# Optimization experiments

Hardware: AMD Instinct MI355X
Metric: run time of the kernel (lower is better)

Reference implementation:

```python
import jax, jax.numpy as jnp
import numpy as np

R = 16
ALPHA = 32
SCALING = ALPHA / R  # 2.0


def setup_inputs() -> dict:
    key = jax.random.key(0)
    k_x, k_w, k_b, k_a, k_bm = jax.random.split(key, 5)
    d = 1024
    x = jax.random.normal(k_x, (4, 4096, d), dtype=jnp.float32)
    W = jax.random.normal(k_w, (d, d), dtype=jnp.float32) * 0.02
    b = jax.random.normal(k_b, (d,), dtype=jnp.float32) * 0.02
    A = jax.random.normal(k_a, (R, d), dtype=jnp.float32) * 0.02
    B = jax.random.normal(k_bm, (d, R), dtype=jnp.float32) * 0.02
    return {"x": x, "W": W, "b": b, "A": A, "B": B}


def reference(x, W, b, A, B):
    # base linear: x @ W^T + b   (W: [out, in])
    base = jnp.einsum("bsd,od->bso", x, W) + b
    # low-rank update: (x @ A^T) @ B^T, scaled (dropout p=0 -> identity)
    u = jnp.einsum("bsd,rd->bsr", x, A)   # [B, S, r]
    update = jnp.einsum("bsr,or->bso", u, B)
    return base + SCALING * update
```

## Files before the change

### kernel.cpp

```cpp
#include <hip/hip_runtime.h>


typedef __bf16 bf16x8 __attribute__((ext_vector_type(8)));
typedef float f32x4 __attribute__((ext_vector_type(4)));
typedef unsigned short ushort8 __attribute__((ext_vector_type(8)));

__device__ __forceinline__ unsigned short f2bf(float f) {
    __bf16 h = (__bf16)f;
    union { __bf16 b; unsigned short u; } v; v.b = h; return v.u;
}
__device__ __forceinline__ ushort8 cvt8u(f32x4 a, f32x4 b) {
    ushort8 o;
#pragma unroll
    for (int i = 0; i < 4; ++i) { o[i] = f2bf(a[i]); o[i + 4] = f2bf(b[i]); }
    return o;
}
__device__ __forceinline__ bf16x8 cvt8(f32x4 a, f32x4 b) {
    union { ushort8 u; bf16x8 h; } v; v.u = cvt8u(a, b); return v.h;
}
__device__ __forceinline__ void gld16(const void* g, void* l) {
    __builtin_amdgcn_global_load_lds(
        (const __attribute__((address_space(1))) unsigned int*)g,
        (__attribute__((address_space(3))) unsigned int*)l, 16, 0, 0);
}

#define FENCE() asm volatile("" ::: "memory")
#define BARRIER() do { FENCE(); __builtin_amdgcn_s_barrier(); FENCE(); } while (0)

__global__ __launch_bounds__(256) void prep(
    const float* __restrict__ W, const float* __restrict__ A,
    const float* __restrict__ B, unsigned short* __restrict__ Weff)
{
    const int idx = blockIdx.x * 256 + threadIdx.x;
    const int o  = idx >> 7;
    const int kc = (idx & 127) << 3;
    float br[16];
#pragma unroll
    for (int r = 0; r < 16; ++r) br[r] = 2.0f * B[o * 16 + r];
    float acc[8];
    const float* wrow = W + (size_t)o * 1024 + kc;
#pragma unroll
    for (int j = 0; j < 8; ++j) acc[j] = wrow[j];
#pragma unroll
    for (int r = 0; r < 16; ++r) {
        const float* arow = A + r * 1024 + kc;
#pragma unroll
        for (int j = 0; j < 8; ++j) acc[j] += br[r] * arow[j];
    }
    ushort8 o8;
#pragma unroll
    for (int j = 0; j < 8; ++j) o8[j] = f2bf(acc[j]);
    *(ushort8*)(Weff + (size_t)o * 1024 + kc) = o8;
}

__global__ __launch_bounds__(512, 4) void gemm256(
    const float* __restrict__ Xf,
    const unsigned short* __restrict__ Wt,
    const float* __restrict__ bias,
    float* __restrict__ out)
{
    extern __shared__ __align__(16) char lds[];

    const int t    = threadIdx.x;
    const int lane = t & 63;
    const int w    = t >> 6;
    const int wr   = w & 3;
    const int wc   = w >> 2;
    const int r16  = lane & 15;
    const int quad = lane >> 4;

    const int nwg = gridDim.x;
    int swz = blockIdx.x;
    if ((nwg & 7) == 0) swz = (swz & 7) * (nwg >> 3) + (swz >> 3);
    const int bm = (swz >> 2) * 128;
    const int bn = (swz & 3) * 256;

    const int ar = t >> 3;
    const int ac = (t & 7) ^ (ar & 7);
    const float* gA = Xf + (size_t)(bm + ar) * 1024 + ac * 4;
    const int adst = t * 16;

    const int brw = t >> 2;
    const int bcc = (t & 3) ^ ((brw >> 1) & 3);
    const unsigned short* pB0 = Wt + (size_t)(bn + brw) * 1024 + bcc * 8;
    const unsigned short* pB1 = pB0 + 131072;
    const int bdst = t * 16;

    const int o0 = ((2 * quad) ^ (r16 & 7)) * 16;
    const int o1 = ((2 * quad + 1) ^ (r16 & 7)) * 16;
    const int hA0 = ((wr * 2 + 0) * 16 + r16) * 128;
    const int hA1 = ((wr * 2 + 1) * 16 + r16) * 128;
    const int bB0 = 16384 + (wc * 16 + r16) * 64 + (quad ^ ((r16 >> 1) & 3)) * 16;

    f32x4 acc[2][8];
#pragma unroll
    for (int i = 0; i < 2; ++i)
#pragma unroll
        for (int jj = 0; jj < 8; ++jj)
            acc[i][jj] = (f32x4){0.f, 0.f, 0.f, 0.f};

#define STAGE_A(BUF, K)                                                        \
    do { gld16(gA + (K),             lds + (BUF) + adst);                      \
         gld16(gA + 65536 + (K),     lds + (BUF) + 8192 + adst);               \
         FENCE(); } while (0)
#define STAGE_B0(BUF, K) do { gld16(pB0 + (K), lds + (BUF) + 16384 + bdst); FENCE(); } while (0)
#define STAGE_B1(BUF, K) do { gld16(pB1 + (K), lds + (BUF) + 24576 + bdst); FENCE(); } while (0)

    STAGE_A(0, 0);
    STAGE_B0(0, 0);
    STAGE_B1(0, 0);
    STAGE_A(32768, 32);
    STAGE_B0(32768, 32);
    asm volatile("s_waitcnt vmcnt(3)" ::: "memory");
    BARRIER();

#pragma unroll 2
    for (int j = 0; j < 32; ++j) {
        const int cur = (j & 1) * 32768;
        const int nxt = cur ^ 32768;

        f32x4 a0l = *(const f32x4*)(lds + cur + hA0 + o0);
        f32x4 a0h = *(const f32x4*)(lds + cur + hA0 + o1);
        f32x4 a1l = *(const f32x4*)(lds + cur + hA1 + o0);
        f32x4 a1h = *(const f32x4*)(lds + cur + hA1 + o1);
        bf16x8 fb[4];
#pragma unroll
        for (int nt = 0; nt < 4; ++nt)
            fb[nt] = *(const bf16x8*)(lds + cur + bB0 + nt * 2048);
        if (j < 31) STAGE_B1(nxt, (j + 1) * 32);
        BARRIER();
        asm volatile("s_waitcnt lgkmcnt(0)" ::: "memory");
        __builtin_amdgcn_sched_barrier(0);
        __builtin_amdgcn_s_setprio(1);
        bf16x8 fa0 = cvt8(a0l, a0h), fa1 = cvt8(a1l, a1h);
#pragma unroll
        for (int nt = 0; nt < 4; ++nt) {
            acc[0][nt] = __builtin_amdgcn_mfma_f32_16x16x32_bf16(fa0, fb[nt], acc[0][nt], 0, 0, 0);
            acc[1][nt] = __builtin_amdgcn_mfma_f32_16x16x32_bf16(fa1, fb[nt], acc[1][nt], 0, 0, 0);
        }
        __builtin_amdgcn_s_setprio(0);
        BARRIER();

#pragma unroll
        for (int nt = 0; nt < 4; ++nt)
            fb[nt] = *(const bf16x8*)(lds + cur + bB0 + 8192 + nt * 2048);
        if (j < 30) { STAGE_A(cur, (j + 2) * 32); STAGE_B0(cur, (j + 2) * 32); }
        if (j < 30)       asm volatile("s_waitcnt vmcnt(3)" ::: "memory");
        else if (j == 30) asm volatile("s_waitcnt vmcnt(0)" ::: "memory");
        BARRIER();
        asm volatile("s_waitcnt lgkmcnt(0)" ::: "memory");
        __builtin_amdgcn_sched_barrier(0);
        __builtin_amdgcn_s_setprio(1);
#pragma unroll
        for (int nt = 0; nt < 4; ++nt) {
            acc[0][nt + 4] = __builtin_amdgcn_mfma_f32_16x16x32_bf16(fa0, fb[nt], acc[0][nt + 4], 0, 0, 0);
            acc[1][nt + 4] = __builtin_amdgcn_mfma_f32_16x16x32_bf16(fa1, fb[nt], acc[1][nt + 4], 0, 0, 0);
        }
        __builtin_amdgcn_s_setprio(0);
        BARRIER();
    }
#undef STAGE_A
#undef STAGE_B0
#undef STAGE_B1

    const int orow0 = bm + wr * 32 + quad * 4;
    const int ocol0 = bn + wc * 16 + r16;
#pragma unroll
    for (int nt = 0; nt < 8; ++nt) {
        const float bv = bias[ocol0 + nt * 32];
#pragma unroll
        for (int mt = 0; mt < 2; ++mt) {
            float* orow = out + (size_t)(orow0 + mt * 16) * 1024 + (ocol0 + nt * 32);
#pragma unroll
            for (int i = 0; i < 4; ++i)
                orow[(size_t)i * 1024] = acc[mt][nt][i] + bv;
        }
    }
}

template <bool XF32>
__global__ __launch_bounds__(256) void gemm_bt(
    const void* __restrict__ X_, const unsigned short* __restrict__ Wt,
    const float* __restrict__ bias, float* __restrict__ out)
{
    __shared__ __align__(16) unsigned short lA[128 * 32];
    __shared__ __align__(16) unsigned short lB[128 * 32];

    const int t    = threadIdx.x;
    const int lane = t & 63;
    const int w    = t >> 6;
    const int bm   = blockIdx.x * 128;
    const int bn   = blockIdx.y * 128;
    const int wm   = (w & 1) * 64;
    const int wn   = (w >> 1) * 64;
    const int r16  = lane & 15;
    const int quad = lane >> 4;

    const int srow = t >> 2;
    const int gc   = (t & 3) ^ ((srow >> 1) & 3);
    unsigned short* lsA = lA + t * 8;
    unsigned short* lsB = lB + t * 8;
    const size_t ga0 = (size_t)(bm + srow) * 1024 + gc * 8;
    const size_t ga1 = (size_t)(bm + srow + 64) * 1024 + gc * 8;
    const unsigned short* gB0 = Wt + (size_t)(bn + srow) * 1024 + gc * 8;

    const int p    = (quad ^ ((r16 >> 1) & 3)) * 8;
    const int aoff = (wm + r16) * 32 + p;
    const int boff = (wn + r16) * 32 + p;

    const unsigned short* Xb = (const unsigned short*)X_;
    const float*          Xf = (const float*)X_;

    f32x4 acc[4][4];
#pragma unroll
    for (int i = 0; i < 4; ++i)
#pragma unroll
        for (int j = 0; j < 4; ++j) {
            f32x4 z = {0.f, 0.f, 0.f, 0.f};
            acc[i][j] = z;
        }

    for (int kt = 0; kt < 1024; kt += 32) {
        if (XF32) {
            f32x4 a0 = *(const f32x4*)(Xf + ga0 + kt);
            f32x4 a1 = *(const f32x4*)(Xf + ga0 + kt + 4);
            f32x4 a2 = *(const f32x4*)(Xf + ga1 + kt);
            f32x4 a3 = *(const f32x4*)(Xf + ga1 + kt + 4);
            *(ushort8*)lsA          = cvt8u(a0, a1);
            *(ushort8*)(lsA + 2048) = cvt8u(a2, a3);
        } else {
            gld16(Xb + ga0 + kt, lsA);
            gld16(Xb + ga1 + kt, lsA + 2048);
        }
        gld16(gB0 + kt,             lsB);
        gld16(gB0 + kt + 64 * 1024, lsB + 2048);
        __syncthreads();

        bf16x8 fa[4], fb[4];
#pragma unroll
        for (int mt = 0; mt < 4; ++mt) fa[mt] = *(const bf16x8*)(lA + aoff + mt * 16 * 32);
#pragma unroll
        for (int nt = 0; nt < 4; ++nt) fb[nt] = *(const bf16x8*)(lB + boff + nt * 16 * 32);

#pragma unroll
        for (int mt = 0; mt < 4; ++mt)
#pragma unroll
            for (int nt = 0; nt < 4; ++nt)
                acc[mt][nt] = __builtin_amdgcn_mfma_f32_16x16x32_bf16(
                    fa[mt], fb[nt], acc[mt][nt], 0, 0, 0);

        __syncthreads();
    }

    const int orow0 = bm + wm + quad * 4;
    const int ocol0 = bn + wn + r16;
#pragma unroll
    for (int nt = 0; nt < 4; ++nt) {
        const float bv = bias[ocol0 + nt * 16];
#pragma unroll
        for (int mt = 0; mt < 4; ++mt)
#pragma unroll
            for (int i = 0; i < 4; ++i)
                out[(size_t)(orow0 + mt * 16 + i) * 1024 + (ocol0 + nt * 16)] =
                    acc[mt][nt][i] + bv;
    }
}

extern "C" void kernel_launch(void* const* d_in, const int* in_sizes, int n_in,
                              void* d_out, int out_size, void* d_ws, size_t ws_size,
                              hipStream_t stream) {
    const float* x  = (const float*)d_in[0];
    const float* W  = (const float*)d_in[1];
    const float* b  = (const float*)d_in[2];
    const float* A  = (const float*)d_in[3];
    const float* Bm = (const float*)d_in[4];
    float* out = (float*)d_out;

    const int M = in_sizes[0] / 1024;

    const bool fast = (ws_size >= (2u << 20) + 4096) && (M % 128 == 0);
    unsigned short* Weff = (unsigned short*)d_ws;
    hipLaunchKernelGGL(prep, dim3(512), dim3(256), 0, stream, W, A, Bm, Weff);
    if (fast) {
        hipLaunchKernelGGL(gemm256, dim3((M / 128) * 4), dim3(512), 65536, stream,
                           x, Weff, b, out);
    } else {
        hipLaunchKernelGGL((gemm_bt<true>), dim3(M / 128, 8), dim3(256), 0, stream,
                           (const void*)x, Weff, b, out);
    }
}
```

Baseline: 168.8 us.

## Pre-convert X to bf16 in prep kernel and retile GEMM to 128x128

The prep kernel now also converts the fp32 activations to bf16 in workspace. The GEMM then streams bf16 X through global-to-LDS loads with K-steps of 64 instead of converting fp32 on the fly. The GEMM tile changes from 128x256 to 128x128 with twice as many workgroups, and LDS fragment layout and swizzle are adjusted to match. This halves the X bytes read inside the GEMM and removes in-loop conversion. In exchange it adds an extra full pass over X (read fp32, write bf16) and reloads W tiles more often.

```diff
diff --git a/kernel.cpp b/kernel.cpp
--- a/kernel.cpp
+++ b/kernel.cpp
@@ -14,9 +14,6 @@
 #pragma unroll
     for (int i = 0; i < 4; ++i) { o[i] = f2bf(a[i]); o[i + 4] = f2bf(b[i]); }
     return o;
-}
-__device__ __forceinline__ bf16x8 cvt8(f32x4 a, f32x4 b) {
-    union { ushort8 u; bf16x8 h; } v; v.u = cvt8u(a, b); return v.h;
 }
 __device__ __forceinline__ void gld16(const void* g, void* l) {
     __builtin_amdgcn_global_load_lds(
@@ -28,33 +25,42 @@
 #define BARRIER() do { FENCE(); __builtin_amdgcn_s_barrier(); FENCE(); } while (0)
 
 __global__ __launch_bounds__(256) void prep(
-    const float* __restrict__ W, const float* __restrict__ A,
-    const float* __restrict__ B, unsigned short* __restrict__ Weff)
+    const float* __restrict__ X, const float* __restrict__ W,
+    const float* __restrict__ A, const float* __restrict__ B,
+    unsigned short* __restrict__ xbf, unsigned short* __restrict__ Weff)
 {
-    const int idx = blockIdx.x * 256 + threadIdx.x;
-    const int o  = idx >> 7;
-    const int kc = (idx & 127) << 3;
-    float br[16];
-#pragma unroll
-    for (int r = 0; r < 16; ++r) br[r] = 2.0f * B[o * 16 + r];
-    float acc[8];
-    const float* wrow = W + (size_t)o * 1024 + kc;
-#pragma unroll
-    for (int j = 0; j < 8; ++j) acc[j] = wrow[j];
-#pragma unroll
-    for (int r = 0; r < 16; ++r) {
-        const float* arow = A + r * 1024 + kc;
-#pragma unroll
-        for (int j = 0; j < 8; ++j) acc[j] += br[r] * arow[j];
-    }
-    ushort8 o8;
-#pragma unroll
-    for (int j = 0; j < 8; ++j) o8[j] = f2bf(acc[j]);
-    *(ushort8*)(Weff + (size_t)o * 1024 + kc) = o8;
+    const int b = blockIdx.x;
+    if (b < 512) {
+        const int idx = b * 256 + threadIdx.x;
+        const int o  = idx >> 7;
+        const int kc = (idx & 127) << 3;
+        float br[16];
+#pragma unroll
+        for (int r = 0; r < 16; ++r) br[r] = 2.0f * B[o * 16 + r];
+        float acc[8];
+        const float* wrow = W + (size_t)o * 1024 + kc;
+#pragma unroll
+        for (int j = 0; j < 8; ++j) acc[j] = wrow[j];
+#pragma unroll
+        for (int r = 0; r < 16; ++r) {
+            const float* arow = A + r * 1024 + kc;
+#pragma unroll
+            for (int j = 0; j < 8; ++j) acc[j] += br[r] * arow[j];
+        }
+        ushort8 o8;
+#pragma unroll
+        for (int j = 0; j < 8; ++j) o8[j] = f2bf(acc[j]);
+        *(ushort8*)(Weff + (size_t)o * 1024 + kc) = o8;
+    } else {
+        const size_t i = ((size_t)(b - 512) * 256 + threadIdx.x) * 8;
+        f32x4 a = *(const f32x4*)(X + i);
+        f32x4 c = *(const f32x4*)(X + i + 4);
+        *(ushort8*)(xbf + i) = cvt8u(a, c);
+    }
 }
 
 __global__ __launch_bounds__(512, 4) void gemm256(
-    const float* __restrict__ Xf,
+    const unsigned short* __restrict__ Xb,
     const unsigned short* __restrict__ Wt,
     const float* __restrict__ bias,
     float* __restrict__ out)
@@ -72,105 +78,111 @@
     const int nwg = gridDim.x;
     int swz = blockIdx.x;
     if ((nwg & 7) == 0) swz = (swz & 7) * (nwg >> 3) + (swz >> 3);
-    const int bm = (swz >> 2) * 128;
-    const int bn = (swz & 3) * 256;
+    const int bm = (swz >> 3) * 128;
+    const int bn = (swz & 7) * 128;
 
     const int ar = t >> 3;
     const int ac = (t & 7) ^ (ar & 7);
-    const float* gA = Xf + (size_t)(bm + ar) * 1024 + ac * 4;
+    const unsigned short* gA = Xb + (size_t)(bm + ar) * 1024 + ac * 8;
+    const unsigned short* gB = Wt + (size_t)(bn + ar) * 1024 + ac * 8;
     const int adst = t * 16;
 
-    const int brw = t >> 2;
-    const int bcc = (t & 3) ^ ((brw >> 1) & 3);
-    const unsigned short* pB0 = Wt + (size_t)(bn + brw) * 1024 + bcc * 8;
-    const unsigned short* pB1 = pB0 + 131072;
-    const int bdst = t * 16;
-
-    const int o0 = ((2 * quad) ^ (r16 & 7)) * 16;
-    const int o1 = ((2 * quad + 1) ^ (r16 & 7)) * 16;
-    const int hA0 = ((wr * 2 + 0) * 16 + r16) * 128;
-    const int hA1 = ((wr * 2 + 1) * 16 + r16) * 128;
-    const int bB0 = 16384 + (wc * 16 + r16) * 64 + (quad ^ ((r16 >> 1) & 3)) * 16;
-
-    f32x4 acc[2][8];
+    const int sw0 = ((quad) ^ (r16 & 7)) * 16;
+    const int sw1 = sw0 ^ 64;
+    const int aB  = wr * 2048 + r16 * 128;
+    const int bB  = 16384 + wc * 2048 + r16 * 128;
+
+    f32x4 acc[2][4];
 #pragma unroll
     for (int i = 0; i < 2; ++i)
 #pragma unroll
-        for (int jj = 0; jj < 8; ++jj)
+        for (int jj = 0; jj < 4; ++jj)
             acc[i][jj] = (f32x4){0.f, 0.f, 0.f, 0.f};
 
-#define STAGE_A(BUF, K)                                                        \
-    do { gld16(gA + (K),             lds + (BUF) + adst);                      \
-         gld16(gA + 65536 + (K),     lds + (BUF) + 8192 + adst);               \
-         FENCE(); } while (0)
-#define STAGE_B0(BUF, K) do { gld16(pB0 + (K), lds + (BUF) + 16384 + bdst); FENCE(); } while (0)
-#define STAGE_B1(BUF, K) do { gld16(pB1 + (K), lds + (BUF) + 24576 + bdst); FENCE(); } while (0)
-
-    STAGE_A(0, 0);
-    STAGE_B0(0, 0);
-    STAGE_B1(0, 0);
-    STAGE_A(32768, 32);
-    STAGE_B0(32768, 32);
+#define STAGE_Aa(BUF, K) do { gld16(gA + (K),         lds + (BUF) + adst);         FENCE(); } while (0)
+#define STAGE_Ab(BUF, K) do { gld16(gA + 65536 + (K), lds + (BUF) + 8192 + adst);  FENCE(); } while (0)
+#define STAGE_B0(BUF, K) do { gld16(gB + (K),         lds + (BUF) + 16384 + adst); FENCE(); } while (0)
+#define STAGE_B1(BUF, K) do { gld16(gB + 65536 + (K), lds + (BUF) + 24576 + adst); FENCE(); } while (0)
+
+    STAGE_Aa(0, 0);  STAGE_Ab(0, 0);  STAGE_B0(0, 0);  STAGE_B1(0, 0);
+    STAGE_Aa(32768, 64);  STAGE_Ab(32768, 64);  STAGE_B0(32768, 64);
     asm volatile("s_waitcnt vmcnt(3)" ::: "memory");
     BARRIER();
 
 #pragma unroll 2
-    for (int j = 0; j < 32; ++j) {
+    for (int j = 0; j < 16; ++j) {
         const int cur = (j & 1) * 32768;
         const int nxt = cur ^ 32768;
-
-        f32x4 a0l = *(const f32x4*)(lds + cur + hA0 + o0);
-        f32x4 a0h = *(const f32x4*)(lds + cur + hA0 + o1);
-        f32x4 a1l = *(const f32x4*)(lds + cur + hA1 + o0);
-        f32x4 a1h = *(const f32x4*)(lds + cur + hA1 + o1);
-        bf16x8 fb[4];
-#pragma unroll
-        for (int nt = 0; nt < 4; ++nt)
-            fb[nt] = *(const bf16x8*)(lds + cur + bB0 + nt * 2048);
-        if (j < 31) STAGE_B1(nxt, (j + 1) * 32);
+        const char* Lb = lds + cur;
+
+        bf16x8 fa[2][2], fb[4][2];
+
+#pragma unroll
+        for (int mt = 0; mt < 2; ++mt) {
+            fa[mt][0] = *(const bf16x8*)(Lb + aB + mt * 8192 + sw0);
+            fa[mt][1] = *(const bf16x8*)(Lb + aB + mt * 8192 + sw1);
+        }
+#pragma unroll
+        for (int nt = 0; nt < 2; ++nt) {
+            fb[nt][0] = *(const bf16x8*)(Lb + bB + nt * 4096 + sw0);
+            fb[nt][1] = *(const bf16x8*)(Lb + bB + nt * 4096 + sw1);
+        }
+        if (j < 15) STAGE_B1(nxt, (j + 1) * 64);
         BARRIER();
         asm volatile("s_waitcnt lgkmcnt(0)" ::: "memory");
         __builtin_amdgcn_sched_barrier(0);
         __builtin_amdgcn_s_setprio(1);
-        bf16x8 fa0 = cvt8(a0l, a0h), fa1 = cvt8(a1l, a1h);
-#pragma unroll
-        for (int nt = 0; nt < 4; ++nt) {
-            acc[0][nt] = __builtin_amdgcn_mfma_f32_16x16x32_bf16(fa0, fb[nt], acc[0][nt], 0, 0, 0);
-            acc[1][nt] = __builtin_amdgcn_mfma_f32_16x16x32_bf16(fa1, fb[nt], acc[1][nt], 0, 0, 0);
-        }
+#pragma unroll
+        for (int mt = 0; mt < 2; ++mt)
+#pragma unroll
+            for (int nt = 0; nt < 2; ++nt)
+#pragma unroll
+                for (int ks = 0; ks < 2; ++ks)
+                    acc[mt][nt] = __builtin_amdgcn_mfma_f32_16x16x32_bf16(
+                        fa[mt][ks], fb[nt][ks], acc[mt][nt], 0, 0, 0);
         __builtin_amdgcn_s_setprio(0);
         BARRIER();
 
 #pragma unroll
-        for (int nt = 0; nt < 4; ++nt)
-            fb[nt] = *(const bf16x8*)(lds + cur + bB0 + 8192 + nt * 2048);
-        if (j < 30) { STAGE_A(cur, (j + 2) * 32); STAGE_B0(cur, (j + 2) * 32); }
-        if (j < 30)       asm volatile("s_waitcnt vmcnt(3)" ::: "memory");
-        else if (j == 30) asm volatile("s_waitcnt vmcnt(0)" ::: "memory");
+        for (int nt = 2; nt < 4; ++nt) {
+            fb[nt][0] = *(const bf16x8*)(Lb + bB + 8192 + (nt - 2) * 4096 + sw0);
+            fb[nt][1] = *(const bf16x8*)(Lb + bB + 8192 + (nt - 2) * 4096 + sw1);
+        }
+        if (j < 14) {
+            STAGE_Aa(cur, (j + 2) * 64);
+            STAGE_Ab(cur, (j + 2) * 64);
+            STAGE_B0(cur, (j + 2) * 64);
+        }
+        if (j < 14)       asm volatile("s_waitcnt vmcnt(3)" ::: "memory");
+        else if (j == 14) asm volatile("s_waitcnt vmcnt(0)" ::: "memory");
         BARRIER();
         asm volatile("s_waitcnt lgkmcnt(0)" ::: "memory");
         __builtin_amdgcn_sched_barrier(0);
         __builtin_amdgcn_s_setprio(1);
 #pragma unroll
-        for (int nt = 0; nt < 4; ++nt) {
-            acc[0][nt + 4] = __builtin_amdgcn_mfma_f32_16x16x32_bf16(fa0, fb[nt], acc[0][nt + 4], 0, 0, 0);
-            acc[1][nt + 4] = __builtin_amdgcn_mfma_f32_16x16x32_bf16(fa1, fb[nt], acc[1][nt + 4], 0, 0, 0);
-        }
+        for (int mt = 0; mt < 2; ++mt)
+#pragma unroll
+            for (int nt = 2; nt < 4; ++nt)
+#pragma unroll
+                for (int ks = 0; ks < 2; ++ks)
+                    acc[mt][nt] = __builtin_amdgcn_mfma_f32_16x16x32_bf16(
+                        fa[mt][ks], fb[nt][ks], acc[mt][nt], 0, 0, 0);
         __builtin_amdgcn_s_setprio(0);
         BARRIER();
     }
-#undef STAGE_A
+#undef STAGE_Aa
+#undef STAGE_Ab
 #undef STAGE_B0
 #undef STAGE_B1
 
-    const int orow0 = bm + wr * 32 + quad * 4;
+    const int orow0 = bm + wr * 16 + quad * 4;
     const int ocol0 = bn + wc * 16 + r16;
 #pragma unroll
-    for (int nt = 0; nt < 8; ++nt) {
+    for (int nt = 0; nt < 4; ++nt) {
         const float bv = bias[ocol0 + nt * 32];
 #pragma unroll
         for (int mt = 0; mt < 2; ++mt) {
-            float* orow = out + (size_t)(orow0 + mt * 16) * 1024 + (ocol0 + nt * 32);
+            float* orow = out + (size_t)(orow0 + mt * 64) * 1024 + (ocol0 + nt * 32);
 #pragma unroll
             for (int i = 0; i < 4; ++i)
                 orow[(size_t)i * 1024] = acc[mt][nt][i] + bv;
@@ -278,13 +290,19 @@
 
     const int M = in_sizes[0] / 1024;
 
-    const bool fast = (ws_size >= (2u << 20) + 4096) && (M % 128 == 0);
-    unsigned short* Weff = (unsigned short*)d_ws;
-    hipLaunchKernelGGL(prep, dim3(512), dim3(256), 0, stream, W, A, Bm, Weff);
+    const bool fast = (ws_size >= ((size_t)(M)*1024*2 + (2u << 20) + 4096)) &&
+                      (M % 128 == 0);
     if (fast) {
-        hipLaunchKernelGGL(gemm256, dim3((M / 128) * 4), dim3(512), 65536, stream,
-                           x, Weff, b, out);
+        unsigned short* xbf  = (unsigned short*)d_ws;
+        unsigned short* Weff = xbf + (size_t)M * 1024;
+        hipLaunchKernelGGL(prep, dim3(512 + M / 2), dim3(256), 0, stream,
+                           x, W, A, Bm, xbf, Weff);
+        hipLaunchKernelGGL(gemm256, dim3((M / 128) * 8), dim3(512), 65536, stream,
+                           xbf, Weff, b, out);
     } else {
+        unsigned short* Weff = (unsigned short*)d_ws;
+        hipLaunchKernelGGL(prep, dim3(512), dim3(256), 0, stream,
+                           x, W, A, Bm, (unsigned short*)nullptr, Weff);
         hipLaunchKernelGGL((gemm_bt<true>), dim3(M / 128, 8), dim3(256), 0, stream,
                            (const void*)x, Weff, b, out);
     }
```

After: 155.1 us. 1.09x faster.
